# Optimization experiments

Hardware: AMD Instinct MI355X
Metric: run time of the kernel (lower is better)

## Reference

```python
import jax, jax.numpy as jnp
import numpy as np

A, B, T = 8, 1024, 32          # agents, batch(envs), time
OBS, ACT, H, HEADS = 64, 16, 128, 4
D = H // HEADS                  # attend_dim = 32
IDIM = OBS + ACT


def setup_inputs() -> dict:
    key = jax.random.key(0)
    ks = jax.random.split(key, 14)
    s = 0.05
    return {
        "obs": jax.random.normal(ks[0], (A, B, T, OBS), jnp.float32),
        "u": jax.random.uniform(ks[1], (A, B, T, ACT), jnp.float32),
        # per-agent critic encoders (enc_fc1)
        "enc_W": jax.random.normal(ks[2], (A, IDIM, H), jnp.float32) * s,
        "enc_b": jax.random.normal(ks[3], (A, H), jnp.float32) * s,
        # per-agent state encoders (s_enc_fc1)
        "s_W": jax.random.normal(ks[4], (A, OBS, H), jnp.float32) * s,
        "s_b": jax.random.normal(ks[5], (A, H), jnp.float32) * s,
        # shared per-head extractors
        "key_W": jax.random.normal(ks[6], (HEADS, H, D), jnp.float32) * s,
        "sel_W": jax.random.normal(ks[7], (HEADS, H, D), jnp.float32) * s,
        "val_W": jax.random.normal(ks[8], (HEADS, H, D), jnp.float32) * s,
        "val_b": jax.random.normal(ks[9], (HEADS, D), jnp.float32) * s,
        # per-agent critic heads
        "crit_W1": jax.random.normal(ks[10], (A, 2 * H, H), jnp.float32) * s,
        "crit_b1": jax.random.normal(ks[11], (A, H), jnp.float32) * s,
        "crit_W2": jax.random.normal(ks[12], (A, H, ACT), jnp.float32) * s,
        "crit_b2": jax.random.normal(ks[13], (A, ACT), jnp.float32) * s,
    }


def reference(obs, u, enc_W, enc_b, s_W, s_b, key_W, sel_W, val_W, val_b,
              crit_W1, crit_b1, crit_W2, crit_b2):
    lrelu = jax.nn.leaky_relu  # torch default negative_slope=0.01
    inp = jnp.concatenate([obs, u], axis=-1)                       # [A,B,T,IDIM]
    sa = lrelu(jnp.einsum('abti,aih->abth', inp, enc_W) + enc_b[:, None, None, :])
    se = lrelu(jnp.einsum('abto,aoh->abth', obs, s_W) + s_b[:, None, None, :])
    # per-head keys/values over sa-encodings; selectors over state encodings
    keys = jnp.einsum('abth,ehd->eabtd', sa, key_W)                # [E,A,B,T,D]
    vals = lrelu(jnp.einsum('abth,ehd->eabtd', sa, val_W) + val_b[:, None, None, None, :])
    sel = jnp.einsum('abth,ehd->eabtd', se, sel_W)
    # self-exclusion attention: agent i attends to all j != i (masked softmax)
    logits = jnp.einsum('eibtd,ejbtd->eijbt', sel, keys) * (1.0 / np.sqrt(D))
    self_mask = jnp.eye(A, dtype=bool)[None, :, :, None, None]
    w = jax.nn.softmax(jnp.where(self_mask, -1e9, logits), axis=2)  # [E,A,A,B,T]
    other = jnp.einsum('eijbt,ejbtd->eibtd', w, vals)               # [E,A,B,T,D]
    other = jnp.moveaxis(other, 0, 3).reshape(A, B, T, H)           # concat heads
    critic_in = jnp.concatenate([se, other], axis=-1)               # [A,B,T,2H]
    h1 = lrelu(jnp.einsum('abtc,ach->abth', critic_in, crit_W1) + crit_b1[:, None, None, :])
    all_q = jnp.einsum('abth,aho->abto', h1, crit_W2) + crit_b2[:, None, None, :]
    idx = jnp.argmax(u, axis=-1, keepdims=True)                     # chosen action
    q = jnp.take_along_axis(all_q, idx, axis=-1)                    # [A,B,T,1]
    return q
```

## Files before the change

kernel.cpp:

```cpp
#include <hip/hip_runtime.h>

namespace {
constexpr int NA = 8, BT = 32768, NOBS = 64, NACT = 16, NH = 128;
constexpr int TOK = 16, NTHREADS = 512;
constexpr int OFF_ENC = 0;
constexpr int OFF_S   = 98304;
constexpr int OFF_KEY = 163840;
constexpr int OFF_SEL = 180224;
constexpr int OFF_VAL = 196608;
constexpr int OFF_C1  = 212992;
constexpr int OFF_C2  = 475136;
constexpr int WT_TOTAL = 491520;
constexpr int WENC = 0, WS_ = 13312, ESCR = 22528, ENC_LDS = 27648;
constexpr int WK = 0, WS = 16384, KOFF = 32768, SOFF = 53248, ATTN_LDS = 73728;
}

typedef short short8 __attribute__((ext_vector_type(8)));
typedef float f32x4 __attribute__((ext_vector_type(4)));
typedef unsigned short u16;

__device__ u16 g_wt[WT_TOTAL];
__device__ u16 g_sa[(size_t)NA * BT * NH];
__device__ u16 g_ci[(size_t)NA * BT * 2 * NH];

__device__ __forceinline__ u16 f2b(float x) {
  unsigned b = __float_as_uint(x);
  return (u16)((b + 0x7FFFu + ((b >> 16) & 1u)) >> 16);
}
__device__ __forceinline__ float b2f(u16 h) { return __uint_as_float(((unsigned)h) << 16); }
__device__ __forceinline__ float lrelu(float x) { return x > 0.0f ? x : 0.01f * x; }
__device__ __forceinline__ short8 ld8(const u16* p) { return *reinterpret_cast<const short8*>(p); }
__device__ __forceinline__ void st8(u16* p, short8 v) { *reinterpret_cast<short8*>(p) = v; }
__device__ __forceinline__ short8 pk8(float4 p, float4 q) {
  short8 r;
  r[0] = (short)f2b(p.x); r[1] = (short)f2b(p.y); r[2] = (short)f2b(p.z); r[3] = (short)f2b(p.w);
  r[4] = (short)f2b(q.x); r[5] = (short)f2b(q.y); r[6] = (short)f2b(q.z); r[7] = (short)f2b(q.w);
  return r;
}

__global__ void maac_wt(const float* __restrict__ encW, const float* __restrict__ sW,
                        const float* __restrict__ keyW, const float* __restrict__ selW,
                        const float* __restrict__ valW, const float* __restrict__ cW1,
                        const float* __restrict__ cW2) {
  for (int i = blockIdx.x * blockDim.x + threadIdx.x; i < WT_TOTAL; i += gridDim.x * blockDim.x) {
    float v; int o = i;
    if (o < OFF_S) {
      int a = o / 12288, r = o % 12288, n = r / 96, k = r % 96;
      v = (k < 80) ? encW[a * 10240 + k * 128 + n] : 0.0f;
    } else if (o < OFF_KEY) {
      int q = o - OFF_S; int a = q / 8192, r = q % 8192, n = r / 64, k = r % 64;
      v = sW[a * 8192 + k * 128 + n];
    } else if (o < OFF_SEL) {
      int q = o - OFF_KEY; int n = q / 128, k = q % 128;
      v = keyW[(n >> 5) * 4096 + k * 32 + (n & 31)];
    } else if (o < OFF_VAL) {
      int q = o - OFF_SEL; int n = q / 128, k = q % 128;
      v = selW[(n >> 5) * 4096 + k * 32 + (n & 31)];
    } else if (o < OFF_C1) {
      int q = o - OFF_VAL; int n = q / 128, k = q % 128;
      v = valW[(n >> 5) * 4096 + k * 32 + (n & 31)];
    } else if (o < OFF_C2) {
      int q = o - OFF_C1; int a = q / 32768, r = q % 32768, n = r / 256, k = r % 256;
      v = cW1[a * 32768 + k * 128 + n];
    } else {
      int q = o - OFF_C2; int a = q / 2048, r = q % 2048, n = r / 128, k = r % 128;
      v = cW2[a * 2048 + k * 16 + n];
    }
    g_wt[i] = f2b(v);
  }
}

__global__ __launch_bounds__(NTHREADS) void maac_enc(
    const float* __restrict__ g_obs, const float* __restrict__ g_u,
    const float* __restrict__ g_encb, const float* __restrict__ g_sb) {
  __shared__ __align__(16) u16 lds[ENC_LDS];

  const int tid = threadIdx.x;
  const int a = blockIdx.y;
  const int tok0 = blockIdx.x * 128;

  for (int z = tid * 8; z < 12288; z += NTHREADS * 8) {
    int row = z / 96, k = z - row * 96;
    st8(&lds[WENC + row * 104 + k], ld8(&g_wt[OFF_ENC + a * 12288 + z]));
  }
  for (int z = tid * 8; z < 8192; z += NTHREADS * 8) {
    int row = z >> 6, k = z & 63;
    st8(&lds[WS_ + row * 72 + k], ld8(&g_wt[OFF_S + a * 8192 + z]));
  }
  __syncthreads();

  const int wv = tid >> 6, l = tid & 63, lr = l & 15, lg = l >> 4;
  const int g0 = tok0 + wv * 16;
  const int scrw = ESCR + wv * 640;

  short8 afr0, afr1, afr2;
  {
    const float4* o4 = reinterpret_cast<const float4*>(g_obs + ((size_t)a * BT + g0 + lr) * NOBS);
    afr0 = pk8(o4[lg * 2], o4[lg * 2 + 1]);
    afr1 = pk8(o4[8 + lg * 2], o4[8 + lg * 2 + 1]);
    if (lg < 2) {
      const float4* u4 = reinterpret_cast<const float4*>(g_u + ((size_t)a * BT + g0 + lr) * NACT);
      afr2 = pk8(u4[lg * 2], u4[lg * 2 + 1]);
    } else {
      afr2 = short8{0, 0, 0, 0, 0, 0, 0, 0};
    }
  }

  #pragma unroll
  for (int g = 0; g < 4; ++g) {
    #pragma unroll
    for (int ntl = 0; ntl < 2; ++ntl) {
      const int nt = 2 * g + ntl;
      f32x4 acc = {0.f, 0.f, 0.f, 0.f};
      const u16* wr = &lds[WENC + (nt * 16 + lr) * 104 + lg * 8];
      acc = __builtin_amdgcn_mfma_f32_16x16x32_bf16(afr0, ld8(wr), acc, 0, 0, 0);
      acc = __builtin_amdgcn_mfma_f32_16x16x32_bf16(afr1, ld8(wr + 32), acc, 0, 0, 0);
      acc = __builtin_amdgcn_mfma_f32_16x16x32_bf16(afr2, ld8(wr + 64), acc, 0, 0, 0);
      float bias = g_encb[a * NH + nt * 16 + lr];
      #pragma unroll
      for (int r = 0; r < 4; ++r)
        lds[scrw + (4 * lg + r) * 40 + ntl * 16 + lr] = f2b(lrelu(acc[r] + bias));
    }
    st8(&g_sa[((size_t)a * BT + g0 + lr) * NH + g * 32 + lg * 8],
        ld8(&lds[scrw + lr * 40 + lg * 8]));
  }
  #pragma unroll
  for (int g = 0; g < 4; ++g) {
    #pragma unroll
    for (int ntl = 0; ntl < 2; ++ntl) {
      const int nt = 2 * g + ntl;
      f32x4 acc = {0.f, 0.f, 0.f, 0.f};
      const u16* wr = &lds[WS_ + (nt * 16 + lr) * 72 + lg * 8];
      acc = __builtin_amdgcn_mfma_f32_16x16x32_bf16(afr0, ld8(wr), acc, 0, 0, 0);
      acc = __builtin_amdgcn_mfma_f32_16x16x32_bf16(afr1, ld8(wr + 32), acc, 0, 0, 0);
      float bias = g_sb[a * NH + nt * 16 + lr];
      #pragma unroll
      for (int r = 0; r < 4; ++r)
        lds[scrw + (4 * lg + r) * 40 + ntl * 16 + lr] = f2b(lrelu(acc[r] + bias));
    }
    st8(&g_ci[((size_t)a * BT + g0 + lr) * 256 + g * 32 + lg * 8],
        ld8(&lds[scrw + lr * 40 + lg * 8]));
  }
}

__global__ __launch_bounds__(NTHREADS) void maac_attn(const float* __restrict__ g_valb) {
  __shared__ __align__(16) u16 lds[ATTN_LDS];

  const int tid = threadIdx.x;
  const int g0 = blockIdx.x * TOK;
  const int a = tid >> 6, l = tid & 63, lr = l & 15, lg = l >> 4;

  for (int z = tid * 8; z < 16384; z += NTHREADS * 8) {
    int n = z >> 7, c = z & 127;
    int cs = c ^ ((n & 7) * 8);
    st8(&lds[WK + n * 128 + cs], ld8(&g_wt[OFF_KEY + z]));
    st8(&lds[WS + n * 128 + cs], ld8(&g_wt[OFF_SEL + z]));
  }

  short8 safr[4], sefr[4];
  #pragma unroll
  for (int ks = 0; ks < 4; ++ks) {
    safr[ks] = ld8(&g_sa[((size_t)a * BT + g0 + lr) * NH + ks * 32 + lg * 8]);
    sefr[ks] = ld8(&g_ci[((size_t)a * BT + g0 + lr) * 256 + ks * 32 + lg * 8]);
  }
  __syncthreads();

  #pragma unroll
  for (int nt = 0; nt < 8; ++nt) {
    const int e = nt >> 1, d = (nt & 1) * 16 + lr;
    const int swz = (lr & 7) * 8;
    const u16* wk = &lds[WK + (nt * 16 + lr) * 128];
    const u16* ws = &lds[WS + (nt * 16 + lr) * 128];
    f32x4 ak = {0.f, 0.f, 0.f, 0.f}, as_ = {0.f, 0.f, 0.f, 0.f};
    #pragma unroll
    for (int ks = 0; ks < 4; ++ks) {
      const int col = (ks * 32 + lg * 8) ^ swz;
      ak  = __builtin_amdgcn_mfma_f32_16x16x32_bf16(safr[ks], ld8(wk + col), ak, 0, 0, 0);
      as_ = __builtin_amdgcn_mfma_f32_16x16x32_bf16(sefr[ks], ld8(ws + col), as_, 0, 0, 0);
    }
    #pragma unroll
    for (int r = 0; r < 4; ++r) {
      const int row = (e * 8 + a) * 16 + 4 * lg + r;
      lds[KOFF + row * 40 + d] = f2b(ak[r]);
      lds[SOFF + row * 40 + d] = f2b(as_[r]);
    }
  }
  __syncthreads();

  float w[NA];
  {
    const int e = tid >> 7, i = (tid >> 4) & 7, t = tid & 15;
    float selv[32];
    #pragma unroll
    for (int q = 0; q < 4; ++q) {
      short8 s = ld8(&lds[SOFF + ((e * 8 + i) * 16 + t) * 40 + q * 8]);
      #pragma unroll
      for (int z = 0; z < 8; ++z) selv[q * 8 + z] = b2f((u16)s[z]);
    }
    float lgt[NA];
    #pragma unroll
    for (int j = 0; j < NA; ++j) {
      float acc = 0.f;
      #pragma unroll
      for (int q = 0; q < 4; ++q) {
        short8 k8 = ld8(&lds[KOFF + ((e * 8 + j) * 16 + t) * 40 + q * 8]);
        #pragma unroll
        for (int z = 0; z < 8; ++z) acc = fmaf(selv[q * 8 + z], b2f((u16)k8[z]), acc);
      }
      lgt[j] = (j == i) ? -1e9f : acc * 0.17677669529663687f;
    }
    float m = lgt[0];
    #pragma unroll
    for (int j = 1; j < NA; ++j) m = fmaxf(m, lgt[j]);
    float s = 0.f;
    #pragma unroll
    for (int j = 0; j < NA; ++j) { lgt[j] = __expf(lgt[j] - m); s += lgt[j]; }
    float inv = 1.f / s;
    #pragma unroll
    for (int j = 0; j < NA; ++j) w[j] = lgt[j] * inv;
  }
  __syncthreads();

  for (int z = tid * 8; z < 16384; z += NTHREADS * 8) {
    int n = z >> 7, c = z & 127;
    int cs = c ^ ((n & 7) * 8);
    st8(&lds[KOFF + n * 128 + cs], ld8(&g_wt[OFF_VAL + z]));
  }
  __syncthreads();

  #pragma unroll
  for (int nt = 0; nt < 8; ++nt) {
    const int e = nt >> 1, d = (nt & 1) * 16 + lr;
    const int swz = (lr & 7) * 8;
    const u16* wr = &lds[KOFF + (nt * 16 + lr) * 128];
    f32x4 acc = {0.f, 0.f, 0.f, 0.f};
    #pragma unroll
    for (int ks = 0; ks < 4; ++ks) {
      const int col = (ks * 32 + lg * 8) ^ swz;
      acc = __builtin_amdgcn_mfma_f32_16x16x32_bf16(safr[ks], ld8(wr + col), acc, 0, 0, 0);
    }
    float bias = g_valb[nt * 16 + lr];
    #pragma unroll
    for (int r = 0; r < 4; ++r) {
      const int row = (e * 8 + a) * 16 + 4 * lg + r;
      lds[SOFF + row * 40 + d] = f2b(lrelu(acc[r] + bias));
    }
  }
  __syncthreads();

  {
    const int e = tid >> 7, i = (tid >> 4) & 7, t = tid & 15;
    float ov[32];
    #pragma unroll
    for (int d = 0; d < 32; ++d) ov[d] = 0.f;
    #pragma unroll
    for (int j = 0; j < NA; ++j) {
      float wj = w[j];
      #pragma unroll
      for (int q = 0; q < 4; ++q) {
        short8 v = ld8(&lds[SOFF + ((e * 8 + j) * 16 + t) * 40 + q * 8]);
        #pragma unroll
        for (int z = 0; z < 8; ++z) ov[q * 8 + z] = fmaf(wj, b2f((u16)v[z]), ov[q * 8 + z]);
      }
    }
    u16* dst = &g_ci[((size_t)i * BT + g0 + t) * 256 + 128 + e * 32];
    #pragma unroll
    for (int q = 0; q < 4; ++q) {
      short8 s;
      #pragma unroll
      for (int z = 0; z < 8; ++z) s[z] = (short)f2b(ov[q * 8 + z]);
      st8(dst + q * 8, s);
    }
  }
}

__global__ __launch_bounds__(NTHREADS) __attribute__((amdgpu_waves_per_eu(4)))
void maac_crit(const float* __restrict__ g_u, const float* __restrict__ g_cb1,
               const float* __restrict__ g_cb2, float* __restrict__ g_out) {
  __shared__ __align__(16) u16 w1[128 * 264];
  __shared__ __align__(16) u16 scr[5120];
  __shared__ int s_idx[128];

  const int tid = threadIdx.x;
  const int a = blockIdx.y;
  const int tok0 = blockIdx.x * 128;

  if (tid < 128) {
    const float* up = g_u + ((size_t)a * BT + tok0 + tid) * NACT;
    int best = 0; float bv = up[0];
    #pragma unroll
    for (int o = 1; o < NACT; ++o) { float v = up[o]; if (v > bv) { bv = v; best = o; } }
    s_idx[tid] = best;
  }
  for (int z = tid * 8; z < 128 * 256; z += NTHREADS * 8) {
    int n = z >> 8, k = z & 255;
    st8(&w1[n * 264 + k], ld8(&g_wt[OFF_C1 + a * 32768 + n * 256 + k]));
  }
  __syncthreads();

  const int wv = tid >> 6, l = tid & 63, lr = l & 15, lg = l >> 4;
  const int g0 = tok0 + wv * 16;
  const int scrw = wv * 640;

  short8 cf[8];
  #pragma unroll
  for (int ks = 0; ks < 8; ++ks)
    cf[ks] = ld8(&g_ci[((size_t)a * BT + g0 + lr) * 256 + ks * 32 + lg * 8]);

  short8 h1fr[4];
  #pragma unroll
  for (int g = 0; g < 4; ++g) {
    #pragma unroll
    for (int ntl = 0; ntl < 2; ++ntl) {
      const int nt = 2 * g + ntl;
      f32x4 acc = {0.f, 0.f, 0.f, 0.f};
      const u16* wr = &w1[(nt * 16 + lr) * 264 + lg * 8];
      #pragma unroll
      for (int ks = 0; ks < 8; ++ks)
        acc = __builtin_amdgcn_mfma_f32_16x16x32_bf16(cf[ks], ld8(wr + ks * 32), acc, 0, 0, 0);
      float bias = g_cb1[a * NH + nt * 16 + lr];
      #pragma unroll
      for (int r = 0; r < 4; ++r)
        scr[scrw + (4 * lg + r) * 40 + ntl * 16 + lr] = f2b(lrelu(acc[r] + bias));
    }
    h1fr[g] = ld8(&scr[scrw + lr * 40 + lg * 8]);
  }

  {
    f32x4 acc = {0.f, 0.f, 0.f, 0.f};
    const u16* wr = g_wt + OFF_C2 + a * 2048 + lr * 128 + lg * 8;
    #pragma unroll
    for (int ks = 0; ks < 4; ++ks)
      acc = __builtin_amdgcn_mfma_f32_16x16x32_bf16(h1fr[ks], ld8(wr + ks * 32), acc, 0, 0, 0);
    float bias = g_cb2[a * NACT + lr];
    #pragma unroll
    for (int r = 0; r < 4; ++r) {
      int t = 4 * lg + r;
      if ((int)lr == s_idx[wv * 16 + t])
        g_out[(size_t)a * BT + g0 + t] = acc[r] + bias;
    }
  }
}

extern "C" void kernel_launch(void* const* d_in, const int* in_sizes, int n_in,
                              void* d_out, int out_size, void* d_ws, size_t ws_size,
                              hipStream_t stream) {
  (void)in_sizes; (void)n_in; (void)d_ws; (void)ws_size; (void)out_size;
  const float* obs  = (const float*)d_in[0];
  const float* u    = (const float*)d_in[1];
  const float* encW = (const float*)d_in[2];
  const float* encb = (const float*)d_in[3];
  const float* sW   = (const float*)d_in[4];
  const float* sb   = (const float*)d_in[5];
  const float* keyW = (const float*)d_in[6];
  const float* selW = (const float*)d_in[7];
  const float* valW = (const float*)d_in[8];
  const float* valb = (const float*)d_in[9];
  const float* cW1  = (const float*)d_in[10];
  const float* cb1  = (const float*)d_in[11];
  const float* cW2  = (const float*)d_in[12];
  const float* cb2  = (const float*)d_in[13];

  hipLaunchKernelGGL(maac_wt, dim3(1920), dim3(256), 0, stream,
                     encW, sW, keyW, selW, valW, cW1, cW2);
  hipLaunchKernelGGL(maac_enc, dim3(BT / 128, NA), dim3(NTHREADS), 0, stream,
                     obs, u, encb, sb);
  hipLaunchKernelGGL(maac_attn, dim3(BT / TOK), dim3(NTHREADS), 0, stream, valb);
  hipLaunchKernelGGL(maac_crit, dim3(BT / 128, NA), dim3(NTHREADS), 0, stream,
                     u, cb1, cb2, (float*)d_out);
}
```

Baseline: 225.7 us.

## Process attention heads in two passes to halve LDS footprint

The attention kernel now handles the four heads in two passes of two heads each. It stages half of the key/selector/value weights and half of the per-head K/S tiles at a time, which shrinks LDS from about 147KB to about 74KB per block so more blocks can be resident on a CU. The cost is extra barriers, re-running the staging loops per pass, and only half the threads doing the softmax and weighted-sum phases.

```diff
diff --git a/kernel.cpp b/kernel.cpp
--- a/kernel.cpp
+++ b/kernel.cpp
@@ -12,7 +12,7 @@
 constexpr int OFF_C2  = 475136;
 constexpr int WT_TOTAL = 491520;
 constexpr int WENC = 0, WS_ = 13312, ESCR = 22528, ENC_LDS = 27648;
-constexpr int WK = 0, WS = 16384, KOFF = 32768, SOFF = 53248, ATTN_LDS = 73728;
+constexpr int WK2 = 0, WS2 = 8192, KOFF2 = 16384, SOFF2 = 26624, ATTN_LDS = 36864;
 }
 
 typedef short short8 __attribute__((ext_vector_type(8)));
@@ -150,127 +150,134 @@
   const int g0 = blockIdx.x * TOK;
   const int a = tid >> 6, l = tid & 63, lr = l & 15, lg = l >> 4;
 
-  for (int z = tid * 8; z < 16384; z += NTHREADS * 8) {
-    int n = z >> 7, c = z & 127;
-    int cs = c ^ ((n & 7) * 8);
-    st8(&lds[WK + n * 128 + cs], ld8(&g_wt[OFF_KEY + z]));
-    st8(&lds[WS + n * 128 + cs], ld8(&g_wt[OFF_SEL + z]));
-  }
-
   short8 safr[4], sefr[4];
   #pragma unroll
   for (int ks = 0; ks < 4; ++ks) {
     safr[ks] = ld8(&g_sa[((size_t)a * BT + g0 + lr) * NH + ks * 32 + lg * 8]);
     sefr[ks] = ld8(&g_ci[((size_t)a * BT + g0 + lr) * 256 + ks * 32 + lg * 8]);
   }
-  __syncthreads();
-
-  #pragma unroll
-  for (int nt = 0; nt < 8; ++nt) {
-    const int e = nt >> 1, d = (nt & 1) * 16 + lr;
-    const int swz = (lr & 7) * 8;
-    const u16* wk = &lds[WK + (nt * 16 + lr) * 128];
-    const u16* ws = &lds[WS + (nt * 16 + lr) * 128];
-    f32x4 ak = {0.f, 0.f, 0.f, 0.f}, as_ = {0.f, 0.f, 0.f, 0.f};
-    #pragma unroll
-    for (int ks = 0; ks < 4; ++ks) {
-      const int col = (ks * 32 + lg * 8) ^ swz;
-      ak  = __builtin_amdgcn_mfma_f32_16x16x32_bf16(safr[ks], ld8(wk + col), ak, 0, 0, 0);
-      as_ = __builtin_amdgcn_mfma_f32_16x16x32_bf16(sefr[ks], ld8(ws + col), as_, 0, 0, 0);
-    }
-    #pragma unroll
-    for (int r = 0; r < 4; ++r) {
-      const int row = (e * 8 + a) * 16 + 4 * lg + r;
-      lds[KOFF + row * 40 + d] = f2b(ak[r]);
-      lds[SOFF + row * 40 + d] = f2b(as_[r]);
-    }
-  }
-  __syncthreads();
-
-  float w[NA];
-  {
-    const int e = tid >> 7, i = (tid >> 4) & 7, t = tid & 15;
-    float selv[32];
-    #pragma unroll
-    for (int q = 0; q < 4; ++q) {
-      short8 s = ld8(&lds[SOFF + ((e * 8 + i) * 16 + t) * 40 + q * 8]);
-      #pragma unroll
-      for (int z = 0; z < 8; ++z) selv[q * 8 + z] = b2f((u16)s[z]);
-    }
-    float lgt[NA];
-    #pragma unroll
-    for (int j = 0; j < NA; ++j) {
-      float acc = 0.f;
+
+  for (int ep = 0; ep < 2; ++ep) {
+    for (int z = tid * 8; z < 8192; z += NTHREADS * 8) {
+      int rl = z >> 7, c = z & 127;
+      int cs = c ^ ((rl & 7) * 8);
+      st8(&lds[WK2 + rl * 128 + cs], ld8(&g_wt[OFF_KEY + ep * 8192 + z]));
+      st8(&lds[WS2 + rl * 128 + cs], ld8(&g_wt[OFF_SEL + ep * 8192 + z]));
+    }
+    __syncthreads();
+
+    #pragma unroll
+    for (int ntL = 0; ntL < 4; ++ntL) {
+      const int eh = ntL >> 1, ntl = ntL & 1;
+      const int d = ntl * 16 + lr;
+      const int rl = eh * 32 + d;
+      const int swz = (lr & 7) * 8;
+      const u16* wk = &lds[WK2 + rl * 128];
+      const u16* ws = &lds[WS2 + rl * 128];
+      f32x4 ak = {0.f, 0.f, 0.f, 0.f}, as_ = {0.f, 0.f, 0.f, 0.f};
+      #pragma unroll
+      for (int ks = 0; ks < 4; ++ks) {
+        const int col = (ks * 32 + lg * 8) ^ swz;
+        ak  = __builtin_amdgcn_mfma_f32_16x16x32_bf16(safr[ks], ld8(wk + col), ak, 0, 0, 0);
+        as_ = __builtin_amdgcn_mfma_f32_16x16x32_bf16(sefr[ks], ld8(ws + col), as_, 0, 0, 0);
+      }
+      #pragma unroll
+      for (int r = 0; r < 4; ++r) {
+        const int row = (eh * 8 + a) * 16 + 4 * lg + r;
+        lds[KOFF2 + row * 40 + d] = f2b(ak[r]);
+        lds[SOFF2 + row * 40 + d] = f2b(as_[r]);
+      }
+    }
+    __syncthreads();
+
+    for (int z = tid * 8; z < 8192; z += NTHREADS * 8) {
+      int rl = z >> 7, c = z & 127;
+      int cs = c ^ ((rl & 7) * 8);
+      st8(&lds[WK2 + rl * 128 + cs], ld8(&g_wt[OFF_VAL + ep * 8192 + z]));
+    }
+
+    float w[NA];
+    if (tid < 256) {
+      const int eh = tid >> 7, i = (tid >> 4) & 7, t = tid & 15;
+      float selv[32];
       #pragma unroll
       for (int q = 0; q < 4; ++q) {
-        short8 k8 = ld8(&lds[KOFF + ((e * 8 + j) * 16 + t) * 40 + q * 8]);
+        short8 s = ld8(&lds[SOFF2 + ((eh * 8 + i) * 16 + t) * 40 + q * 8]);
         #pragma unroll
-        for (int z = 0; z < 8; ++z) acc = fmaf(selv[q * 8 + z], b2f((u16)k8[z]), acc);
-      }
-      lgt[j] = (j == i) ? -1e9f : acc * 0.17677669529663687f;
-    }
-    float m = lgt[0];
-    #pragma unroll
-    for (int j = 1; j < NA; ++j) m = fmaxf(m, lgt[j]);
-    float s = 0.f;
-    #pragma unroll
-    for (int j = 0; j < NA; ++j) { lgt[j] = __expf(lgt[j] - m); s += lgt[j]; }
-    float inv = 1.f / s;
-    #pragma unroll
-    for (int j = 0; j < NA; ++j) w[j] = lgt[j] * inv;
-  }
-  __syncthreads();
-
-  for (int z = tid * 8; z < 16384; z += NTHREADS * 8) {
-    int n = z >> 7, c = z & 127;
-    int cs = c ^ ((n & 7) * 8);
-    st8(&lds[KOFF + n * 128 + cs], ld8(&g_wt[OFF_VAL + z]));
-  }
-  __syncthreads();
-
-  #pragma unroll
-  for (int nt = 0; nt < 8; ++nt) {
-    const int e = nt >> 1, d = (nt & 1) * 16 + lr;
-    const int swz = (lr & 7) * 8;
-    const u16* wr = &lds[KOFF + (nt * 16 + lr) * 128];
-    f32x4 acc = {0.f, 0.f, 0.f, 0.f};
-    #pragma unroll
-    for (int ks = 0; ks < 4; ++ks) {
-      const int col = (ks * 32 + lg * 8) ^ swz;
-      acc = __builtin_amdgcn_mfma_f32_16x16x32_bf16(safr[ks], ld8(wr + col), acc, 0, 0, 0);
-    }
-    float bias = g_valb[nt * 16 + lr];
-    #pragma unroll
-    for (int r = 0; r < 4; ++r) {
-      const int row = (e * 8 + a) * 16 + 4 * lg + r;
-      lds[SOFF + row * 40 + d] = f2b(lrelu(acc[r] + bias));
-    }
-  }
-  __syncthreads();
-
-  {
-    const int e = tid >> 7, i = (tid >> 4) & 7, t = tid & 15;
-    float ov[32];
-    #pragma unroll
-    for (int d = 0; d < 32; ++d) ov[d] = 0.f;
-    #pragma unroll
-    for (int j = 0; j < NA; ++j) {
-      float wj = w[j];
+        for (int z = 0; z < 8; ++z) selv[q * 8 + z] = b2f((u16)s[z]);
+      }
+      float lgt[NA];
+      #pragma unroll
+      for (int j = 0; j < NA; ++j) {
+        float acc = 0.f;
+        #pragma unroll
+        for (int q = 0; q < 4; ++q) {
+          short8 k8 = ld8(&lds[KOFF2 + ((eh * 8 + j) * 16 + t) * 40 + q * 8]);
+          #pragma unroll
+          for (int z = 0; z < 8; ++z) acc = fmaf(selv[q * 8 + z], b2f((u16)k8[z]), acc);
+        }
+        lgt[j] = (j == i) ? -1e9f : acc * 0.17677669529663687f;
+      }
+      float m = lgt[0];
+      #pragma unroll
+      for (int j = 1; j < NA; ++j) m = fmaxf(m, lgt[j]);
+      float s = 0.f;
+      #pragma unroll
+      for (int j = 0; j < NA; ++j) { lgt[j] = __expf(lgt[j] - m); s += lgt[j]; }
+      float inv = 1.f / s;
+      #pragma unroll
+      for (int j = 0; j < NA; ++j) w[j] = lgt[j] * inv;
+    }
+    __syncthreads();
+
+    #pragma unroll
+    for (int ntL = 0; ntL < 4; ++ntL) {
+      const int eh = ntL >> 1, ntl = ntL & 1;
+      const int d = ntl * 16 + lr;
+      const int rl = eh * 32 + d;
+      const int n = (2 * ep + eh) * 32 + d;
+      const int swz = (lr & 7) * 8;
+      const u16* wr = &lds[WK2 + rl * 128];
+      f32x4 acc = {0.f, 0.f, 0.f, 0.f};
+      #pragma unroll
+      for (int ks = 0; ks < 4; ++ks) {
+        const int col = (ks * 32 + lg * 8) ^ swz;
+        acc = __builtin_amdgcn_mfma_f32_16x16x32_bf16(safr[ks], ld8(wr + col), acc, 0, 0, 0);
+      }
+      float bias = g_valb[n];
+      #pragma unroll
+      for (int r = 0; r < 4; ++r) {
+        const int row = (eh * 8 + a) * 16 + 4 * lg + r;
+        lds[SOFF2 + row * 40 + d] = f2b(lrelu(acc[r] + bias));
+      }
+    }
+    __syncthreads();
+
+    if (tid < 256) {
+      const int eh = tid >> 7, i = (tid >> 4) & 7, t = tid & 15;
+      float ov[32];
+      #pragma unroll
+      for (int d = 0; d < 32; ++d) ov[d] = 0.f;
+      #pragma unroll
+      for (int j = 0; j < NA; ++j) {
+        float wj = w[j];
+        #pragma unroll
+        for (int q = 0; q < 4; ++q) {
+          short8 v = ld8(&lds[SOFF2 + ((eh * 8 + j) * 16 + t) * 40 + q * 8]);
+          #pragma unroll
+          for (int z = 0; z < 8; ++z) ov[q * 8 + z] = fmaf(wj, b2f((u16)v[z]), ov[q * 8 + z]);
+        }
+      }
+      u16* dst = &g_ci[((size_t)i * BT + g0 + t) * 256 + 128 + (2 * ep + eh) * 32];
       #pragma unroll
       for (int q = 0; q < 4; ++q) {
-        short8 v = ld8(&lds[SOFF + ((e * 8 + j) * 16 + t) * 40 + q * 8]);
+        short8 s;
         #pragma unroll
-        for (int z = 0; z < 8; ++z) ov[q * 8 + z] = fmaf(wj, b2f((u16)v[z]), ov[q * 8 + z]);
-      }
-    }
-    u16* dst = &g_ci[((size_t)i * BT + g0 + t) * 256 + 128 + e * 32];
-    #pragma unroll
-    for (int q = 0; q < 4; ++q) {
-      short8 s;
-      #pragma unroll
-      for (int z = 0; z < 8; ++z) s[z] = (short)f2b(ov[q * 8 + z]);
-      st8(dst + q * 8, s);
-    }
+        for (int z = 0; z < 8; ++z) s[z] = (short)f2b(ov[q * 8 + z]);
+        st8(dst + q * 8, s);
+      }
+    }
+    __syncthreads();
   }
 }
 
```

After: 246.4 us. 1.09x slower.
